# Kernel optimization log

Hardware: AMD Instinct MI355X
Metric: run time of the kernel (lower is better)

Reference implementation:

```python
import jax, jax.numpy as jnp
import numpy as np

B_SZ, SEQ, H = 8, 1024, 2048
LN_EPS = 1e-6
CLIP = 1.0e6


def setup_inputs() -> dict:
    key = jax.random.key(0)
    ks = jax.random.split(key, 8)
    lecun = 1.0 / np.sqrt(H)
    return {
        "x": jax.random.normal(ks[0], (B_SZ, SEQ, H), dtype=jnp.float32),
        "context": jnp.zeros((B_SZ, H), dtype=jnp.float32),
        # learned params
        "A": -jax.random.uniform(ks[1], (H,), dtype=jnp.float32),  # diagonal decay (zeros-init in src; small negative for stable decay)
        "Bm": jax.random.normal(ks[2], (H, H), dtype=jnp.float32) * lecun,
        "Cm": jax.random.normal(ks[3], (H, H), dtype=jnp.float32) * lecun,
        "dt_kernel": jax.random.normal(ks[4], (H, 1), dtype=jnp.float32) * 0.02,
        "dt_bias": jnp.zeros((1,), dtype=jnp.float32),
        "gate_kernel": jax.random.normal(ks[5], (H, H), dtype=jnp.float32) * lecun,
        "gate_bias": jnp.zeros((H,), dtype=jnp.float32),
        "ln_scale": jnp.ones((H,), dtype=jnp.float32),
        "ln_bias": jnp.zeros((H,), dtype=jnp.float32),
    }


def _layernorm(x, scale, bias):
    mu = jnp.mean(x, axis=-1, keepdims=True)
    var = jnp.mean(jnp.square(x - mu), axis=-1, keepdims=True)
    return (x - mu) * jax.lax.rsqrt(var + LN_EPS) * scale + bias


def reference(x, context, A, Bm, Cm, dt_kernel, dt_bias, gate_kernel, gate_bias, ln_scale, ln_bias):
    xn = jnp.clip(_layernorm(x, ln_scale, ln_bias), -CLIP, CLIP)  # [B,S,H]
    xt = jnp.swapaxes(xn, 0, 1)  # time-major [S,B,H]

    def step(state, x_t):
        # x_t: [B,H]; delta: [B,1] from Dense(1)
        delta = jnp.exp(x_t @ dt_kernel + dt_bias)
        decay = jnp.exp(delta * A)                  # [B,H] via broadcast
        new_state = state * decay + x_t @ Bm        # [B,H]
        out = new_state @ Cm                        # [B,H]
        return new_state, out

    final_state, ys = jax.lax.scan(step, context, xt)
    outputs = jnp.swapaxes(ys, 0, 1)  # [B,S,H]
    gate = outputs @ gate_kernel + gate_bias
    outputs = outputs * jax.nn.sigmoid(gate)  # GLU
    # dropout deterministic (training=False) -> identity
    return outputs, final_state
```

## Files before the change

kernel.cpp:

```cpp
#include <hip/hip_runtime.h>
#include <hip/hip_bf16.h>

#define H_DIM 2048
#define B_SZ  8
#define SEQ   1024
#define M_DIM (B_SZ*SEQ)
#define KDIM  2048
#define NKT   (KDIM/64)
#define CCH   32
#define CLEN  (SEQ/CCH)

using f32x4 = __attribute__((ext_vector_type(4))) float;
using s16x8 = __attribute__((ext_vector_type(8))) short;

__device__ __forceinline__ float bf2f(unsigned short u) {
  unsigned int x = ((unsigned int)u) << 16;
  return __builtin_bit_cast(float, x);
}
__device__ __forceinline__ unsigned short f2bf(float f) {
  unsigned int x = __builtin_bit_cast(unsigned int, f);
  unsigned int r = (x + 0x7fffu + ((x >> 16) & 1u)) >> 16;
  return (unsigned short)r;
}

__device__ __forceinline__ void gl_lds16(const void* g, void* l) {
  __builtin_amdgcn_global_load_lds(
      (__attribute__((address_space(1))) void*)g,
      (__attribute__((address_space(3))) void*)l, 16, 0, 0);
}

__global__ __launch_bounds__(256) void transpose3_kernel(
    const float* __restrict__ s0, unsigned short* __restrict__ d0,
    const float* __restrict__ s1, unsigned short* __restrict__ d1,
    const float* __restrict__ s2, unsigned short* __restrict__ d2)
{
  const float* src = (blockIdx.z == 0) ? s0 : (blockIdx.z == 1) ? s1 : s2;
  unsigned short* dst = (blockIdx.z == 0) ? d0 : (blockIdx.z == 1) ? d1 : d2;
  __shared__ float t[32][33];
  int tx = threadIdx.x & 31, ty = threadIdx.x >> 5;
  int c0 = blockIdx.x << 5, r0 = blockIdx.y << 5;
#pragma unroll
  for (int i = 0; i < 32; i += 8)
    t[ty + i][tx] = src[(size_t)(r0 + ty + i) * H_DIM + (c0 + tx)];
  __syncthreads();
#pragma unroll
  for (int i = 0; i < 32; i += 8)
    dst[(size_t)(c0 + ty + i) * H_DIM + (r0 + tx)] = f2bf(t[tx][ty + i]);
}

__global__ __launch_bounds__(256) void ln_delta_kernel(
    const float* __restrict__ x, const float* __restrict__ lns,
    const float* __restrict__ lnb, const float* __restrict__ dtk,
    const float* __restrict__ dtb, unsigned short* __restrict__ xn,
    float* __restrict__ delta)
{
  const int row = blockIdx.x;
  const int tid = threadIdx.x;
  const float* xr = x + (size_t)row * H_DIM;
  float v[8];
  *(float4*)&v[0] = ((const float4*)xr)[tid * 2];
  *(float4*)&v[4] = ((const float4*)xr)[tid * 2 + 1];
  float s1 = 0.f, s2 = 0.f;
#pragma unroll
  for (int j = 0; j < 8; ++j) { s1 += v[j]; s2 += v[j] * v[j]; }
  __shared__ float red[8];
#pragma unroll
  for (int off = 32; off; off >>= 1) {
    s1 += __shfl_down(s1, off);
    s2 += __shfl_down(s2, off);
  }
  if ((tid & 63) == 0) { red[tid >> 6] = s1; red[4 + (tid >> 6)] = s2; }
  __syncthreads();
  float mean = (red[0] + red[1] + red[2] + red[3]) * (1.0f / H_DIM);
  float var  = (red[4] + red[5] + red[6] + red[7]) * (1.0f / H_DIM) - mean * mean;
  float rstd = rsqrtf(var + 1e-6f);

  float sc[8], bi[8], dk[8];
  *(float4*)&sc[0] = ((const float4*)lns)[tid * 2];
  *(float4*)&sc[4] = ((const float4*)lns)[tid * 2 + 1];
  *(float4*)&bi[0] = ((const float4*)lnb)[tid * 2];
  *(float4*)&bi[4] = ((const float4*)lnb)[tid * 2 + 1];
  *(float4*)&dk[0] = ((const float4*)dtk)[tid * 2];
  *(float4*)&dk[4] = ((const float4*)dtk)[tid * 2 + 1];

  float dot = 0.f;
  s16x8 o;
#pragma unroll
  for (int j = 0; j < 8; ++j) {
    float xv = (v[j] - mean) * rstd * sc[j] + bi[j];
    xv = fminf(fmaxf(xv, -1.0e6f), 1.0e6f);
    dot += xv * dk[j];
    o[j] = (short)f2bf(xv);
  }
  *(s16x8*)(xn + (size_t)row * H_DIM + tid * 8) = o;

  __syncthreads();
#pragma unroll
  for (int off = 32; off; off >>= 1) dot += __shfl_down(dot, off);
  if ((tid & 63) == 0) red[tid >> 6] = dot;
  __syncthreads();
  if (tid == 0)
    delta[row] = __expf(red[0] + red[1] + red[2] + red[3] + dtb[0]);
}

__global__ __launch_bounds__(256) void scan1_kernel(
    const unsigned short* __restrict__ U, const float* __restrict__ delta,
    const float* __restrict__ Adiag, float* __restrict__ Q, float* __restrict__ P)
{
  const int h = blockIdx.x * 1024 + threadIdx.x * 4;
  const int c = blockIdx.y, b = blockIdx.z;
  const float4 a = *(const float4*)(Adiag + h);
  const unsigned short* u = U + ((size_t)b * SEQ + c * CLEN) * H_DIM + h;
  const float* dl = delta + b * SEQ + c * CLEN;
  float4 st = {0.f, 0.f, 0.f, 0.f};
  float4 pr = {1.f, 1.f, 1.f, 1.f};
#pragma unroll 8
  for (int s = 0; s < CLEN; ++s) {
    const float d = dl[s];
    const ushort4 uv = *(const ushort4*)(u + (size_t)s * H_DIM);
    const float dx = __expf(d * a.x), dy = __expf(d * a.y);
    const float dz = __expf(d * a.z), dw = __expf(d * a.w);
    st.x = fmaf(st.x, dx, bf2f(uv.x)); st.y = fmaf(st.y, dy, bf2f(uv.y));
    st.z = fmaf(st.z, dz, bf2f(uv.z)); st.w = fmaf(st.w, dw, bf2f(uv.w));
    pr.x *= dx; pr.y *= dy; pr.z *= dz; pr.w *= dw;
  }
  const size_t idx = ((size_t)b * CCH + c) * H_DIM + h;
  *(float4*)(Q + idx) = st;
  *(float4*)(P + idx) = pr;
}

__global__ __launch_bounds__(256) void scan2_kernel(
    const float* __restrict__ Q, const float* __restrict__ P,
    const float* __restrict__ ctx, float* __restrict__ sIn,
    float* __restrict__ finalSt)
{
  const int h = blockIdx.x * 256 + threadIdx.x;
  const int b = blockIdx.y;
  float s = ctx[b * H_DIM + h];
#pragma unroll
  for (int c = 0; c < CCH; ++c) {
    const size_t idx = ((size_t)b * CCH + c) * H_DIM + h;
    sIn[idx] = s;
    s = fmaf(s, P[idx], Q[idx]);
  }
  finalSt[b * H_DIM + h] = s;
}

__global__ __launch_bounds__(256) void scan3_kernel(
    const unsigned short* __restrict__ U, const float* __restrict__ delta,
    const float* __restrict__ Adiag, const float* __restrict__ sIn,
    unsigned short* __restrict__ states)
{
  const int h = blockIdx.x * 1024 + threadIdx.x * 4;
  const int c = blockIdx.y, b = blockIdx.z;
  const float4 a = *(const float4*)(Adiag + h);
  const unsigned short* u = U + ((size_t)b * SEQ + c * CLEN) * H_DIM + h;
  unsigned short* so = states + ((size_t)b * SEQ + c * CLEN) * H_DIM + h;
  const float* dl = delta + b * SEQ + c * CLEN;
  float4 st = *(const float4*)(sIn + ((size_t)b * CCH + c) * H_DIM + h);
#pragma unroll 8
  for (int s = 0; s < CLEN; ++s) {
    const float d = dl[s];
    const ushort4 uv = *(const ushort4*)(u + (size_t)s * H_DIM);
    const float dx = __expf(d * a.x), dy = __expf(d * a.y);
    const float dz = __expf(d * a.z), dw = __expf(d * a.w);
    st.x = fmaf(st.x, dx, bf2f(uv.x)); st.y = fmaf(st.y, dy, bf2f(uv.y));
    st.z = fmaf(st.z, dz, bf2f(uv.z)); st.w = fmaf(st.w, dw, bf2f(uv.w));
    ushort4 ov = { f2bf(st.x), f2bf(st.y), f2bf(st.z), f2bf(st.w) };
    *(ushort4*)(so + (size_t)s * H_DIM) = ov;
  }
}


#define BARR()  __builtin_amdgcn_s_barrier();
#define VMC(N)  asm volatile("s_waitcnt vmcnt(" #N ")" ::: "memory");

#define RD_A(DST, PL, PHH, OFF) { _Pragma("unroll") for (int i_ = 0; i_ < 4; ++i_) { \
    DST[0][i_] = *(const s16x8*)((PL) + (OFF) + i_ * 4096); \
    DST[1][i_] = *(const s16x8*)((PHH) + (OFF) + i_ * 4096); } }
#define RD_B(DST, PL, PHH, OFF) { _Pragma("unroll") for (int j_ = 0; j_ < 2; ++j_) { \
    DST[0][j_] = *(const s16x8*)((PL) + (OFF) + j_ * 8192); \
    DST[1][j_] = *(const s16x8*)((PHH) + (OFF) + j_ * 8192); } }

#define QMM(IB, JB, AF, BF) { __builtin_amdgcn_s_setprio(1); \
  _Pragma("unroll") for (int i_ = 0; i_ < 4; ++i_) \
  _Pragma("unroll") for (int j_ = 0; j_ < 2; ++j_) { \
    acc[(IB)+i_][(JB)+j_] = __builtin_amdgcn_mfma_f32_16x16x32_bf16(AF[0][i_], BF[0][j_], acc[(IB)+i_][(JB)+j_], 0, 0, 0); \
    acc[(IB)+i_][(JB)+j_] = __builtin_amdgcn_mfma_f32_16x16x32_bf16(AF[1][i_], BF[1][j_], acc[(IB)+i_][(JB)+j_], 0, 0, 0); } \
  __builtin_amdgcn_s_setprio(0); }

#define STAGE_A(BUF, HH, TT) { const char* s_ = srcA + (HH) * 524288 + (TT) * 128; \
  char* d_ = ldsA + (BUF) * 32768 + (HH) * 16384 + tid16; \
  gl_lds16(s_, d_); gl_lds16(s_ + 262144, d_ + 8192); }
#define STAGE_B(BUF, HH, TT) { const char* s_ = srcB + (HH) * 524288 + (TT) * 128; \
  char* d_ = ldsB + (BUF) * 32768 + (HH) * 16384 + tid16; \
  gl_lds16(s_, d_); gl_lds16(s_ + 262144, d_ + 8192); }

template <int EPI>
__global__ __launch_bounds__(512, 2) void gemm8p(
    const char* __restrict__ Ab, const char* __restrict__ Bb,
    float* __restrict__ outF, unsigned short* __restrict__ outH,
    const unsigned short* __restrict__ Ybf, const float* __restrict__ gbias)
{
  extern __shared__ char lds[];
  char* ldsA = lds;
  char* ldsB = lds + 65536;

  const int tid  = threadIdx.x;
  const int lane = tid & 63, wid = tid >> 6;
  const int wr = wid >> 2, wc = wid & 3;
  const int fr = lane & 15, kq = lane >> 4;

  const int bid = blockIdx.x;
  const int xcd = bid & 7;
  const int li  = bid >> 3;
  const int bm  = (xcd >> 1) * 8 + (li & 7);
  const int bn  = (xcd & 1) * 4 + (li >> 3);

  const int grow = tid >> 3;
  const int gswz = ((tid & 7) ^ (grow & 7)) << 4;
  const char* srcA = Ab + ((size_t)(bm * 256 + grow)) * 4096 + gswz;
  const char* srcB = Bb + ((size_t)(bn * 256 + grow)) * 4096 + gswz;
  const int tid16 = tid << 4;

  const int sw0 = ((kq ^ (fr & 7)) << 4);
  const int sw1 = (((4 | kq) ^ (fr & 7)) << 4);
  const char* pa0b0 = ldsA + wr * 2048 + fr * 128 + sw0;
  const char* pa1b0 = ldsA + wr * 2048 + fr * 128 + sw1;
  const char* pa0b1 = pa0b0 + 32768;
  const char* pa1b1 = pa1b0 + 32768;
  const char* pb0b0 = ldsB + wc * 2048 + fr * 128 + sw0;
  const char* pb1b0 = ldsB + wc * 2048 + fr * 128 + sw1;
  const char* pb0b1 = pb0b0 + 32768;
  const char* pb1b1 = pb1b0 + 32768;

  f32x4 acc[8][4] = {};
  s16x8 a03[2][4], a47[2][4], b01a[2][2], b01b[2][2], b23[2][2];

  STAGE_A(0, 0, 0); STAGE_B(0, 0, 0); STAGE_B(0, 1, 0); STAGE_A(0, 1, 0);
  STAGE_A(1, 0, 1); STAGE_B(1, 0, 1); STAGE_B(1, 1, 1);
  VMC(6);
  BARR();
  RD_A(a03, pa0b0, pa1b0, 0);
  RD_B(b01a, pb0b0, pb1b0, 0);

  for (int t = 0; t < NKT / 2 - 1; ++t) {
    const int T0 = 2 * t;
    RD_B(b23, pb0b0, pb1b0, 16384);
    STAGE_A(1, 1, T0 + 1);
    QMM(0, 0, a03, b01a);
    VMC(6); BARR();
    RD_A(a47, pa0b0, pa1b0, 16384);
    STAGE_A(0, 0, T0 + 2);
    QMM(0, 2, a03, b23);
    VMC(6); BARR();
    RD_B(b01b, pb0b1, pb1b1, 0);
    STAGE_B(0, 0, T0 + 2);
    QMM(4, 0, a47, b01a);
    VMC(6); BARR();
    RD_A(a03, pa0b1, pa1b1, 0);
    STAGE_B(0, 1, T0 + 2);
    QMM(4, 2, a47, b23);
    VMC(6); BARR();
    RD_B(b23, pb0b1, pb1b1, 16384);
    STAGE_A(0, 1, T0 + 2);
    QMM(0, 0, a03, b01b);
    VMC(6); BARR();
    RD_A(a47, pa0b1, pa1b1, 16384);
    STAGE_A(1, 0, T0 + 3);
    QMM(0, 2, a03, b23);
    VMC(6); BARR();
    RD_B(b01a, pb0b0, pb1b0, 0);
    STAGE_B(1, 0, T0 + 3);
    QMM(4, 0, a47, b01b);
    VMC(6); BARR();
    RD_A(a03, pa0b0, pa1b0, 0);
    STAGE_B(1, 1, T0 + 3);
    QMM(4, 2, a47, b23);
    VMC(6); BARR();
  }

  RD_B(b23, pb0b0, pb1b0, 16384);
  STAGE_A(1, 1, 31);
  QMM(0, 0, a03, b01a);
  VMC(6); BARR();
  RD_A(a47, pa0b0, pa1b0, 16384);
  QMM(0, 2, a03, b23);
  VMC(0); BARR();
  RD_B(b01b, pb0b1, pb1b1, 0);
  QMM(4, 0, a47, b01a);
  RD_A(a03, pa0b1, pa1b1, 0);
  QMM(4, 2, a47, b23);
  RD_B(b23, pb0b1, pb1b1, 16384);
  QMM(0, 0, a03, b01b);
  RD_A(a47, pa0b1, pa1b1, 16384);
  QMM(0, 2, a03, b23);
  QMM(4, 0, a47, b01b);
  QMM(4, 2, a47, b23);

  __syncthreads();
  const int cr = (lane >> 4) << 2;
  const int cc = lane & 15;
  if constexpr (EPI == 1) {
#pragma unroll
    for (int i = 0; i < 8; ++i)
#pragma unroll
      for (int j = 0; j < 4; ++j)
#pragma unroll
        for (int r = 0; r < 4; ++r) {
          const int row = (2 * i + wr) * 16 + cr + r;
          const int col = (4 * j + wc) * 16 + cc;
          const int off = (row * 512 + col * 2) ^ ((row & 7) << 4);
          *(unsigned short*)(lds + off) = f2bf(acc[i][j][r]);
        }
    __syncthreads();
#pragma unroll
    for (int it = 0; it < 16; ++it) {
      const int L = it * 8192 + tid * 16;
      const int row = L >> 9, inrow = L & 511;
      const s16x8 v = *(const s16x8*)(lds + (L ^ ((row & 7) << 4)));
      *(s16x8*)(outH + ((size_t)(bm * 256 + row)) * H_DIM + bn * 256 + (inrow >> 1)) = v;
    }
  } else {
#pragma unroll
    for (int p = 0; p < 2; ++p) {
      if (p) __syncthreads();
#pragma unroll
      for (int i = 4 * p; i < 4 * p + 4; ++i)
#pragma unroll
        for (int j = 0; j < 4; ++j)
#pragma unroll
          for (int r = 0; r < 4; ++r) {
            const int lrow = (2 * i + wr) * 16 + cr + r - 128 * p;
            const int col = (4 * j + wc) * 16 + cc;
            const int off = (lrow * 1024 + col * 4) ^ ((lrow & 7) << 4);
            *(float*)(lds + off) = acc[i][j][r];
          }
      __syncthreads();
#pragma unroll
      for (int it = 0; it < 16; ++it) {
        const int L = it * 8192 + tid * 16;
        const int lrow = L >> 10, inrow = L & 1023;
        const f32x4 v = *(const f32x4*)(lds + (L ^ ((lrow & 7) << 4)));
        const size_t growg = (size_t)(bm * 256 + 128 * p + lrow);
        const int gcol = bn * 256 + (inrow >> 2);
        const float4 gb4 = *(const float4*)(gbias + gcol);
        const ushort4 y4 = *(const ushort4*)(Ybf + growg * H_DIM + gcol);
        float4 o;
        o.x = bf2f(y4.x) / (1.f + __expf(-(v[0] + gb4.x)));
        o.y = bf2f(y4.y) / (1.f + __expf(-(v[1] + gb4.y)));
        o.z = bf2f(y4.z) / (1.f + __expf(-(v[2] + gb4.z)));
        o.w = bf2f(y4.w) / (1.f + __expf(-(v[3] + gb4.w)));
        *(float4*)(outF + growg * H_DIM + gcol) = o;
      }
    }
  }
}

extern "C" void kernel_launch(void* const* d_in, const int* in_sizes, int n_in,
                              void* d_out, int out_size, void* d_ws, size_t ws_size,
                              hipStream_t stream) {
  (void)in_sizes; (void)n_in; (void)out_size; (void)ws_size;
  const float* x     = (const float*)d_in[0];
  const float* ctx   = (const float*)d_in[1];
  const float* Adiag = (const float*)d_in[2];
  const float* Bm    = (const float*)d_in[3];
  const float* Cm    = (const float*)d_in[4];
  const float* dtk   = (const float*)d_in[5];
  const float* dtb   = (const float*)d_in[6];
  const float* gk    = (const float*)d_in[7];
  const float* gb    = (const float*)d_in[8];
  const float* lns   = (const float*)d_in[9];
  const float* lnb   = (const float*)d_in[10];
  float* outF = (float*)d_out;

  char* ws = (char*)d_ws;
  unsigned short* xnY    = (unsigned short*)ws; ws += (size_t)M_DIM * H_DIM * 2;
  unsigned short* U      = (unsigned short*)ws; ws += (size_t)M_DIM * H_DIM * 2;
  unsigned short* states = (unsigned short*)ws; ws += (size_t)M_DIM * H_DIM * 2;
  unsigned short* T1     = (unsigned short*)ws; ws += (size_t)H_DIM * H_DIM * 2;
  unsigned short* T2     = (unsigned short*)ws; ws += (size_t)H_DIM * H_DIM * 2;
  unsigned short* T3     = (unsigned short*)ws; ws += (size_t)H_DIM * H_DIM * 2;
  float* delta           = (float*)ws;          ws += (size_t)M_DIM * 4;
  float* Qbuf            = (float*)ws;          ws += (size_t)B_SZ * CCH * H_DIM * 4;
  float* Pbuf            = (float*)ws;          ws += (size_t)B_SZ * CCH * H_DIM * 4;
  float* sInBuf          = (float*)ws;          ws += (size_t)B_SZ * CCH * H_DIM * 4;

  hipFuncSetAttribute((const void*)&gemm8p<1>,
                      hipFuncAttributeMaxDynamicSharedMemorySize, 131072);
  hipFuncSetAttribute((const void*)&gemm8p<2>,
                      hipFuncAttributeMaxDynamicSharedMemorySize, 131072);

  dim3 tb(256);
  transpose3_kernel<<<dim3(64, 64, 3), tb, 0, stream>>>(Bm, T1, Cm, T2, gk, T3);
  ln_delta_kernel<<<M_DIM, tb, 0, stream>>>(x, lns, lnb, dtk, dtb, xnY, delta);
  gemm8p<1><<<256, 512, 131072, stream>>>(
      (const char*)xnY, (const char*)T1, nullptr, U, nullptr, nullptr);
  scan1_kernel<<<dim3(H_DIM / 1024, CCH, B_SZ), tb, 0, stream>>>(
      U, delta, Adiag, Qbuf, Pbuf);
  scan2_kernel<<<dim3(H_DIM / 256, B_SZ), tb, 0, stream>>>(
      Qbuf, Pbuf, ctx, sInBuf, outF + (size_t)M_DIM * H_DIM);
  scan3_kernel<<<dim3(H_DIM / 1024, CCH, B_SZ), tb, 0, stream>>>(
      U, delta, Adiag, sInBuf, states);
  gemm8p<1><<<256, 512, 131072, stream>>>(
      (const char*)states, (const char*)T2, nullptr, xnY, nullptr, nullptr);
  gemm8p<2><<<256, 512, 131072, stream>>>(
      (const char*)xnY, (const char*)T3, outF, nullptr, xnY, gb);
}
```

Measured before the change: 257.0 us.

## Restructure GEMM main loop with explicit LDS waits and barrier-fenced MFMA phases

```diff
diff --git a/kernel.cpp b/kernel.cpp
--- a/kernel.cpp
+++ b/kernel.cpp
@@ -173,6 +173,7 @@
 
 
 #define BARR()  __builtin_amdgcn_s_barrier();
+#define LGKM0() asm volatile("s_waitcnt lgkmcnt(0)");
 #define VMC(N)  asm volatile("s_waitcnt vmcnt(" #N ")" ::: "memory");
 
 #define RD_A(DST, PL, PHH, OFF) { _Pragma("unroll") for (int i_ = 0; i_ < 4; ++i_) { \
@@ -235,67 +236,58 @@
   const char* pb1b1 = pb1b0 + 32768;
 
   f32x4 acc[8][4] = {};
-  s16x8 a03[2][4], a47[2][4], b01a[2][2], b01b[2][2], b23[2][2];
+  s16x8 a03[2][4], a47[2][4], b01[2][2], b23[2][2];
 
   STAGE_A(0, 0, 0); STAGE_B(0, 0, 0); STAGE_B(0, 1, 0); STAGE_A(0, 1, 0);
+  VMC(4);
   STAGE_A(1, 0, 1); STAGE_B(1, 0, 1); STAGE_B(1, 1, 1);
   VMC(6);
   BARR();
-  RD_A(a03, pa0b0, pa1b0, 0);
-  RD_B(b01a, pb0b0, pb1b0, 0);
 
   for (int t = 0; t < NKT / 2 - 1; ++t) {
     const int T0 = 2 * t;
+    RD_A(a03, pa0b0, pa1b0, 0);
+    RD_B(b01, pb0b0, pb1b0, 0);
+    STAGE_A(1, 1, T0 + 1);
+    BARR(); LGKM0(); QMM(0, 0, a03, b01); BARR();
     RD_B(b23, pb0b0, pb1b0, 16384);
-    STAGE_A(1, 1, T0 + 1);
-    QMM(0, 0, a03, b01a);
-    VMC(6); BARR();
+    STAGE_A(0, 0, T0 + 2);
+    BARR(); LGKM0(); QMM(0, 2, a03, b23); BARR();
     RD_A(a47, pa0b0, pa1b0, 16384);
-    STAGE_A(0, 0, T0 + 2);
-    QMM(0, 2, a03, b23);
-    VMC(6); BARR();
-    RD_B(b01b, pb0b1, pb1b1, 0);
     STAGE_B(0, 0, T0 + 2);
-    QMM(4, 0, a47, b01a);
-    VMC(6); BARR();
+    BARR(); LGKM0(); QMM(4, 0, a47, b01); BARR();
+    STAGE_B(0, 1, T0 + 2);
+    BARR(); QMM(4, 2, a47, b23); VMC(6); BARR();
     RD_A(a03, pa0b1, pa1b1, 0);
-    STAGE_B(0, 1, T0 + 2);
-    QMM(4, 2, a47, b23);
-    VMC(6); BARR();
+    RD_B(b01, pb0b1, pb1b1, 0);
+    STAGE_A(0, 1, T0 + 2);
+    BARR(); LGKM0(); QMM(0, 0, a03, b01); BARR();
     RD_B(b23, pb0b1, pb1b1, 16384);
-    STAGE_A(0, 1, T0 + 2);
-    QMM(0, 0, a03, b01b);
-    VMC(6); BARR();
+    STAGE_A(1, 0, T0 + 3);
+    BARR(); LGKM0(); QMM(0, 2, a03, b23); BARR();
     RD_A(a47, pa0b1, pa1b1, 16384);
-    STAGE_A(1, 0, T0 + 3);
-    QMM(0, 2, a03, b23);
-    VMC(6); BARR();
-    RD_B(b01a, pb0b0, pb1b0, 0);
     STAGE_B(1, 0, T0 + 3);
-    QMM(4, 0, a47, b01b);
-    VMC(6); BARR();
-    RD_A(a03, pa0b0, pa1b0, 0);
+    BARR(); LGKM0(); QMM(4, 0, a47, b01); BARR();
     STAGE_B(1, 1, T0 + 3);
-    QMM(4, 2, a47, b23);
-    VMC(6); BARR();
-  }
-
+    BARR(); QMM(4, 2, a47, b23); VMC(6); BARR();
+  }
+
+  RD_A(a03, pa0b0, pa1b0, 0);
+  RD_B(b01, pb0b0, pb1b0, 0);
+  STAGE_A(1, 1, 31);
+  BARR(); LGKM0(); QMM(0, 0, a03, b01); BARR();
   RD_B(b23, pb0b0, pb1b0, 16384);
-  STAGE_A(1, 1, 31);
-  QMM(0, 0, a03, b01a);
-  VMC(6); BARR();
+  BARR(); LGKM0(); QMM(0, 2, a03, b23); BARR();
   RD_A(a47, pa0b0, pa1b0, 16384);
+  BARR(); LGKM0(); QMM(4, 0, a47, b01); BARR();
+  BARR(); QMM(4, 2, a47, b23); VMC(0); BARR();
+  RD_A(a03, pa0b1, pa1b1, 0);
+  RD_B(b01, pb0b1, pb1b1, 0);
+  QMM(0, 0, a03, b01);
+  RD_B(b23, pb0b1, pb1b1, 16384);
   QMM(0, 2, a03, b23);
-  VMC(0); BARR();
-  RD_B(b01b, pb0b1, pb1b1, 0);
-  QMM(4, 0, a47, b01a);
-  RD_A(a03, pa0b1, pa1b1, 0);
-  QMM(4, 2, a47, b23);
-  RD_B(b23, pb0b1, pb1b1, 16384);
-  QMM(0, 0, a03, b01b);
   RD_A(a47, pa0b1, pa1b1, 16384);
-  QMM(0, 2, a03, b23);
-  QMM(4, 0, a47, b01b);
+  QMM(4, 0, a47, b01);
   QMM(4, 2, a47, b23);
 
   __syncthreads();
```

Result: no change. 252.5 us (-1.7%).
